# Kernel optimization log

Hardware: AMD Instinct MI355X
Metric: run time of the kernel (lower is better)

Reference implementation:

```python
import jax, jax.numpy as jnp
from jax import lax
import numpy as np

A = 2048          # number of agents
H = 128           # hidden_dim
G = 8             # grid_size
NB = 32.0         # neighbourhood_size
CELL = 2.0 * NB / G


def setup_inputs() -> dict:
    key = jax.random.key(0)
    k1, k2, k3 = jax.random.split(key, 3)
    hidden = jax.random.normal(k1, (A, H), dtype=jnp.float32)
    # positions spread wider than the neighbourhood so bins are exercised
    pos = jax.random.uniform(k2, (A, 2), dtype=jnp.float32, minval=-48.0, maxval=48.0)
    mask = jnp.ones((A,), dtype=bool)
    W = jax.random.normal(k3, (H, G * G * H), dtype=jnp.float32) * (1.0 / np.sqrt(G * G * H))
    b = jnp.zeros((H,), dtype=jnp.float32)
    return {"hidden": hidden, "pos": pos, "mask": mask, "W": W, "b": b}


def reference(hidden, pos, mask, W, b):
    a, h = hidden.shape
    # rel[i, j] = pos[j] - pos[i]  (matches `rel = pos - pos[i]` indexed at j)
    rel = pos[None, :, :] - pos[:, None, :]          # [A, A, 2]
    rx, ry = rel[..., 0], rel[..., 1]
    in_range = (jnp.abs(rx) < NB) & (jnp.abs(ry) < NB)  # also False for NaN rel
    col = jnp.clip(jnp.floor((rx + NB) / CELL).astype(jnp.int32), 0, G - 1)
    row = jnp.clip(jnp.floor((ry + NB) / CELL).astype(jnp.int32), 0, G - 1)
    bins = row * G + col                              # [A, A] in [0, G*G)
    not_self = ~jnp.eye(a, dtype=bool)
    valid = in_range & not_self & mask[None, :]       # [A, A]

    # grid[i, bcell, :] = sum over j with bins[i,j]==bcell of hidden[j]
    def scan_body(_, bcell):
        Mb = (valid & (bins == bcell)).astype(hidden.dtype)   # [A, A]
        return None, Mb @ hidden                              # [A, H]

    _, grid = lax.scan(scan_body, None, jnp.arange(G * G))    # [G*G, A, H]
    grid = jnp.transpose(grid, (1, 0, 2)).reshape(a, G * G * h)
    pooled = grid @ W.T + b                                   # [A, H]

    valid_i = mask & ~jnp.isnan(pos).any(axis=-1)
    return jnp.where(valid_i[:, None], pooled, jnp.zeros_like(pooled))
```

## Files before the change

### kernel.cpp

```cpp
#include <hip/hip_runtime.h>
#include <hip/hip_bf16.h>
#include <stdint.h>


typedef __attribute__((ext_vector_type(4))) float f32x4;
typedef __attribute__((ext_vector_type(8))) short short8;

#define O_HB   0u
#define O_WB   1048576u
#define O_GRID 3145728u
#define O_PART 36700160u
#define O_POSM 36700160u

__device__ __forceinline__ void gl_lds16(const void* g, void* l) {
  __builtin_amdgcn_global_load_lds((const __attribute__((address_space(1))) void*)g,
                                   (__attribute__((address_space(3))) void*)l, 16, 0, 0);
}

__device__ __forceinline__ float bf_lo(uint32_t w) {
  union { uint32_t u; float f; } v{w << 16}; return v.f;
}
__device__ __forceinline__ float bf_hi(uint32_t w) {
  union { uint32_t u; float f; } v{w & 0xffff0000u}; return v.f;
}
__device__ __forceinline__ uint32_t pack_bf2(float x, float y) {
  __hip_bfloat16 bx = __float2bfloat16(x), by = __float2bfloat16(y);
  return ((uint32_t)(*(unsigned short*)&by) << 16) | (*(unsigned short*)&bx);
}

__global__ __launch_bounds__(256) void sp_prep(const float* __restrict__ hidden,
                                               const float* __restrict__ W,
                                               const float* __restrict__ pos,
                                               const int* __restrict__ mask,
                                               __hip_bfloat16* __restrict__ hb,
                                               __hip_bfloat16* __restrict__ wb,
                                               float2* __restrict__ posm) {
  int idx = blockIdx.x * 256 + threadIdx.x;
  const int HID4 = (2049 * 128) / 4;
  const int W4   = (128 * 8192) / 4;
  if (idx < HID4) {
    int e = idx * 4;
    float4 v = make_float4(0.f, 0.f, 0.f, 0.f);
    if (e < 2048 * 128) v = *reinterpret_cast<const float4*>(hidden + e);
    ushort4 pk;
    pk.x = (ushort)(pack_bf2(v.x, v.x) & 0xffffu);
    pk.y = (ushort)(pack_bf2(v.y, v.y) & 0xffffu);
    pk.z = (ushort)(pack_bf2(v.z, v.z) & 0xffffu);
    pk.w = (ushort)(pack_bf2(v.w, v.w) & 0xffffu);
    *reinterpret_cast<ushort4*>(hb + e) = pk;
  } else if (idx < HID4 + W4) {
    int e = (idx - HID4) * 4;
    float4 v = *reinterpret_cast<const float4*>(W + e);
    ushort4 pk;
    pk.x = (ushort)(pack_bf2(v.x, v.x) & 0xffffu);
    pk.y = (ushort)(pack_bf2(v.y, v.y) & 0xffffu);
    pk.z = (ushort)(pack_bf2(v.z, v.z) & 0xffffu);
    pk.w = (ushort)(pack_bf2(v.w, v.w) & 0xffffu);
    *reinterpret_cast<ushort4*>(wb + e) = pk;
  } else {
    int j = idx - (HID4 + W4);
    if (j < 2048) {
      float2 p = reinterpret_cast<const float2*>(pos)[j];
      union { uint32_t u; float f; } qn{0x7fc00000u};
      float2 o;
      bool m = (mask[j] != 0);
      o.x = m ? p.x : qn.f;
      o.y = m ? p.y : qn.f;
      posm[j] = o;
    }
  }
}

__global__ __launch_bounds__(256) void sp_build(const float* __restrict__ pos,
                                                const float2* __restrict__ posm,
                                                const __hip_bfloat16* __restrict__ hb,
                                                __hip_bfloat16* __restrict__ grid) {
  __shared__ __align__(16) uint32_t list32[2560];
  __shared__ int hist[4][64];
  __shared__ int cur[4][64];
  __shared__ int offs[65];
  int t = threadIdx.x;
  int wv = t >> 6;
  int i = blockIdx.x;
  float pxi = pos[2 * i], pyi = pos[2 * i + 1];
  reinterpret_cast<int*>(hist)[t] = 0;
  __syncthreads();
  int bins[8];
  #pragma unroll
  for (int jj = 0; jj < 8; ++jj) {
    int j = t + jj * 256;
    float2 pj = posm[j];
    float rx = pj.x - pxi, ry = pj.y - pyi;
    bool ok = (fabsf(rx) < 32.f) && (fabsf(ry) < 32.f) && (j != i);
    int b = -1;
    if (ok) {
      int col = (int)floorf((rx + 32.f) * 0.125f);
      int row = (int)floorf((ry + 32.f) * 0.125f);
      b = row * 8 + col;
      atomicAdd(&hist[wv][b], 1);
    }
    bins[jj] = b;
  }
  #pragma unroll
  for (int q = 0; q < 10; ++q) {
    int k = t + q * 256;
    if (k < 2560) list32[k] = (2048u << 8);
  }
  __syncthreads();
  if (t < 64) {
    int h0 = hist[0][t], h1 = hist[1][t], h2 = hist[2][t], h3 = hist[3][t];
    int tot = h0 + h1 + h2 + h3;
    int padded = (tot + 7) & ~7;
    int x = padded;
    #pragma unroll
    for (int d = 1; d < 64; d <<= 1) {
      int y = __shfl_up(x, d);
      if (t >= d) x += y;
    }
    offs[t + 1] = x;
    int base = x - padded;
    cur[0][t] = base;
    cur[1][t] = base + h0;
    cur[2][t] = base + h0 + h1;
    cur[3][t] = base + h0 + h1 + h2;
    if (t == 0) offs[0] = 0;
  }
  __syncthreads();
  #pragma unroll
  for (int jj = 0; jj < 8; ++jj) {
    int j = t + jj * 256;
    int b = bins[jj];
    if (b >= 0) { int k = atomicAdd(&cur[wv][b], 1); list32[k] = ((uint32_t)j << 8); }
  }
  __syncthreads();
  int l = t & 63;
  int lq = l & 31;
  int dsh = (l >> 5) << 2;
  int lqoff = lq * 8;
  const char* hbB = reinterpret_cast<const char*>(hb);
  for (int c = wv; c < 64; c += 4) {
    int s0 = offs[c], e0 = offs[c + 1];
    float a0 = 0.f, a1 = 0.f, a2 = 0.f, a3 = 0.f;
    float b0 = 0.f, b1 = 0.f, b2 = 0.f, b3 = 0.f;
    if (s0 < e0) {
      uint4 js = *reinterpret_cast<const uint4*>(&list32[s0 + dsh]);
      uint2 r0 = *reinterpret_cast<const uint2*>(hbB + js.x + lqoff);
      uint2 r1 = *reinterpret_cast<const uint2*>(hbB + js.y + lqoff);
      uint2 r2 = *reinterpret_cast<const uint2*>(hbB + js.z + lqoff);
      uint2 r3 = *reinterpret_cast<const uint2*>(hbB + js.w + lqoff);
      for (int k = s0 + 8; k < e0; k += 8) {
        uint4 jn = *reinterpret_cast<const uint4*>(&list32[k + dsh]);
        uint2 n0 = *reinterpret_cast<const uint2*>(hbB + jn.x + lqoff);
        uint2 n1 = *reinterpret_cast<const uint2*>(hbB + jn.y + lqoff);
        uint2 n2 = *reinterpret_cast<const uint2*>(hbB + jn.z + lqoff);
        uint2 n3 = *reinterpret_cast<const uint2*>(hbB + jn.w + lqoff);
        a0 += bf_lo(r0.x); a1 += bf_hi(r0.x); a2 += bf_lo(r0.y); a3 += bf_hi(r0.y);
        b0 += bf_lo(r1.x); b1 += bf_hi(r1.x); b2 += bf_lo(r1.y); b3 += bf_hi(r1.y);
        a0 += bf_lo(r2.x); a1 += bf_hi(r2.x); a2 += bf_lo(r2.y); a3 += bf_hi(r2.y);
        b0 += bf_lo(r3.x); b1 += bf_hi(r3.x); b2 += bf_lo(r3.y); b3 += bf_hi(r3.y);
        r0 = n0; r1 = n1; r2 = n2; r3 = n3;
      }
      a0 += bf_lo(r0.x); a1 += bf_hi(r0.x); a2 += bf_lo(r0.y); a3 += bf_hi(r0.y);
      b0 += bf_lo(r1.x); b1 += bf_hi(r1.x); b2 += bf_lo(r1.y); b3 += bf_hi(r1.y);
      a0 += bf_lo(r2.x); a1 += bf_hi(r2.x); a2 += bf_lo(r2.y); a3 += bf_hi(r2.y);
      b0 += bf_lo(r3.x); b1 += bf_hi(r3.x); b2 += bf_lo(r3.y); b3 += bf_hi(r3.y);
    }
    float c0 = a0 + b0, c1 = a1 + b1, c2 = a2 + b2, c3 = a3 + b3;
    c0 += __shfl_xor(c0, 32);
    c1 += __shfl_xor(c1, 32);
    c2 += __shfl_xor(c2, 32);
    c3 += __shfl_xor(c3, 32);
    if (l < 32) {
      uint2 pk;
      pk.x = pack_bf2(c0, c1);
      pk.y = pack_bf2(c2, c3);
      *reinterpret_cast<uint2*>(
          reinterpret_cast<char*>(grid) + ((size_t)((i << 6) + c) * 256 + (size_t)lq * 8)) = pk;
    }
  }
}

__global__ __launch_bounds__(256) void sp_gemm(const __hip_bfloat16* __restrict__ Ag,
                                               const __hip_bfloat16* __restrict__ Wb,
                                               float* __restrict__ part) {
  __shared__ __align__(16) char Asm[8192];
  __shared__ __align__(16) char Bsm[16384];
  int t = threadIdx.x;
  int lane = t & 63;
  int w = t >> 6;
  int wm = w >> 1, wn = w & 1;
  int bx = blockIdx.x;
  int mt = bx & 31;
  int sp = bx >> 5;
  int i0 = mt * 64;
  long kbase = (long)sp * 512 * 2;
  const char* Agc = (const char*)Ag;
  const char* Wbc = (const char*)Wb;
  f32x4 acc[2][4] = {};
  for (int st = 0; st < 8; ++st) {
    long kb = kbase + st * 128;
    #pragma unroll
    for (int q = 0; q < 2; ++q) {
      int o = (q * 256 + t) * 16;
      int r = o >> 7;
      int sc = (o & 127) ^ ((r & 7) << 4);
      gl_lds16(Agc + (long)(i0 + r) * 16384 + kb + sc, Asm + o);
    }
    #pragma unroll
    for (int q = 0; q < 4; ++q) {
      int o = (q * 256 + t) * 16;
      int r = o >> 7;
      int sc = (o & 127) ^ ((r & 7) << 4);
      gl_lds16(Wbc + (long)r * 16384 + kb + sc, Bsm + o);
    }
    __syncthreads();
    short8 af[2][2], bfr[4][2];
    #pragma unroll
    for (int fr = 0; fr < 2; ++fr)
      #pragma unroll
      for (int ks = 0; ks < 2; ++ks) {
        int r = wm * 32 + fr * 16 + (lane & 15);
        int g = ks * 4 + (lane >> 4);
        int byt = r * 128 + ((g ^ (r & 7)) << 4);
        af[fr][ks] = *reinterpret_cast<const short8*>(Asm + byt);
      }
    #pragma unroll
    for (int fc = 0; fc < 4; ++fc)
      #pragma unroll
      for (int ks = 0; ks < 2; ++ks) {
        int n = wn * 64 + fc * 16 + (lane & 15);
        int g = ks * 4 + (lane >> 4);
        int byt = n * 128 + ((g ^ (n & 7)) << 4);
        bfr[fc][ks] = *reinterpret_cast<const short8*>(Bsm + byt);
      }
    #pragma unroll
    for (int fr = 0; fr < 2; ++fr)
      #pragma unroll
      for (int fc = 0; fc < 4; ++fc)
        #pragma unroll
        for (int ks = 0; ks < 2; ++ks)
          acc[fr][fc] = __builtin_amdgcn_mfma_f32_16x16x32_bf16(af[fr][ks], bfr[fc][ks],
                                                                acc[fr][fc], 0, 0, 0);
    __syncthreads();
  }
  float* p = part + (long)sp * 262144;
  #pragma unroll
  for (int fr = 0; fr < 2; ++fr)
    #pragma unroll
    for (int fc = 0; fc < 4; ++fc)
      #pragma unroll
      for (int r4 = 0; r4 < 4; ++r4) {
        int ii = i0 + wm * 32 + fr * 16 + (lane >> 4) * 4 + r4;
        int nn = wn * 64 + fc * 16 + (lane & 15);
        p[(long)ii * 128 + nn] = acc[fr][fc][r4];
      }
}

__global__ __launch_bounds__(256) void sp_reduce(const float* __restrict__ part,
                                                 const float* __restrict__ bias,
                                                 const float* __restrict__ pos,
                                                 const int* __restrict__ mask,
                                                 float* __restrict__ out) {
  int g = blockIdx.x * 256 + threadIdx.x;
  int i = g >> 7, n = g & 127;
  float acc = bias[n];
  #pragma unroll
  for (int s = 0; s < 16; ++s) acc += part[(long)s * 262144 + g];
  float px = pos[2 * i], py = pos[2 * i + 1];
  bool vi = (mask[i] != 0) && (px == px) && (py == py);
  out[g] = vi ? acc : 0.f;
}

extern "C" void kernel_launch(void* const* d_in, const int* in_sizes, int n_in,
                              void* d_out, int out_size, void* d_ws, size_t ws_size,
                              hipStream_t stream) {
  const float* hidden  = (const float*)d_in[0];
  const float* pos     = (const float*)d_in[1];
  const int*   mask    = (const int*)d_in[2];
  const float* W       = (const float*)d_in[3];
  const float* bias    = (const float*)d_in[4];
  char* ws = (char*)d_ws;
  __hip_bfloat16* hb   = (__hip_bfloat16*)(ws + O_HB);
  __hip_bfloat16* wb   = (__hip_bfloat16*)(ws + O_WB);
  __hip_bfloat16* grid = (__hip_bfloat16*)(ws + O_GRID);
  float* part          = (float*)(ws + O_PART);
  float2* posm         = (float2*)(ws + O_POSM);
  float* out           = (float*)d_out;

  sp_prep<<<1289, 256, 0, stream>>>(hidden, W, pos, mask, hb, wb, posm);
  sp_build<<<2048, 256, 0, stream>>>(pos, posm, hb, grid);
  sp_gemm<<<512, 256, 0, stream>>>(grid, wb, part);
  sp_reduce<<<1024, 256, 0, stream>>>(part, bias, pos, mask, out);
}
```

Baseline: 67.65 us.

## Give each wavefront one agent with a single streaming pass over per-cell neighbour lists

sp_build now assigns one agent per wavefront (4 agents per block, 512 blocks) instead of one agent per block. Per-wave histograms, prefix scans and 16-bit neighbour lists replace the block-wide shared lists and most __syncthreads. The gather becomes one software-pipelined stream over the whole padded list, flushing a cell whenever a boundary is crossed, so short cells no longer idle the wave. The price is more divergent control flow, a bigger per-wave LDS footprint and serialized boundary handling within each wave.

```diff
diff --git a/kernel.cpp b/kernel.cpp
--- a/kernel.cpp
+++ b/kernel.cpp
@@ -71,112 +71,135 @@
   }
 }
 
+#define FLUSH_CELL()                                                        \
+  {                                                                         \
+    float d0 = a0 + __shfl_xor(a0, 32);                                     \
+    float d1 = a1 + __shfl_xor(a1, 32);                                     \
+    float d2 = a2 + __shfl_xor(a2, 32);                                     \
+    float d3 = a3 + __shfl_xor(a3, 32);                                     \
+    if (loA) {                                                              \
+      uint2 pk; pk.x = pack_bf2(d0, d1); pk.y = pack_bf2(d2, d3);           \
+      *reinterpret_cast<uint2*>(gbase + (c << 8) + laneoff) = pk;           \
+    }                                                                       \
+    a0 = a1 = a2 = a3 = 0.f;                                                \
+  }
+
+#define ISSUE_PAIR(Ldst, sdexpr)                                            \
+  {                                                                         \
+    int sd_ = __builtin_amdgcn_readfirstlane(sdexpr);                       \
+    uint32_t oA_ = (uint32_t)(sd_ & 0xffff) << 8;                           \
+    uint32_t oB_ = ((uint32_t)sd_ >> 16) << 8;                              \
+    uint32_t sel_ = loA ? oA_ : oB_;                                        \
+    Ldst = *reinterpret_cast<const uint2*>(hbB + sel_ + laneoff);           \
+  }
+
+#define ISSUE_BATCH(L, Ea, Eb)                                              \
+  ISSUE_PAIR(L[0], Ea.x) ISSUE_PAIR(L[1], Ea.y)                             \
+  ISSUE_PAIR(L[2], Ea.z) ISSUE_PAIR(L[3], Ea.w)                             \
+  ISSUE_PAIR(L[4], Eb.x) ISSUE_PAIR(L[5], Eb.y)                             \
+  ISSUE_PAIR(L[6], Eb.z) ISSUE_PAIR(L[7], Eb.w)
+
+#define CONSUME_PAIR(Lp)                                                    \
+  {                                                                         \
+    while (c < 64 && rpos == bnd) {                                         \
+      FLUSH_CELL();                                                         \
+      ++c;                                                                  \
+      bnd = (c < 64) ? __builtin_amdgcn_readlane(bndv, c) : 0x7fffffff;     \
+    }                                                                       \
+    uint2 w_ = Lp;                                                          \
+    a0 += bf_lo(w_.x); a1 += bf_hi(w_.x);                                   \
+    a2 += bf_lo(w_.y); a3 += bf_hi(w_.y);                                   \
+    rpos += 2;                                                              \
+  }
+
 __global__ __launch_bounds__(256) void sp_build(const float* __restrict__ pos,
                                                 const float2* __restrict__ posm,
                                                 const __hip_bfloat16* __restrict__ hb,
                                                 __hip_bfloat16* __restrict__ grid) {
-  __shared__ __align__(16) uint32_t list32[2560];
+  __shared__ __align__(16) uint16_t lists[4][2240];
   __shared__ int hist[4][64];
-  __shared__ int cur[4][64];
-  __shared__ int offs[65];
+  __shared__ int curs[4][64];
   int t = threadIdx.x;
   int wv = t >> 6;
-  int i = blockIdx.x;
+  int lane = t & 63;
+  int i = blockIdx.x * 4 + wv;
+  bool loA = lane < 32;
+  uint32_t laneoff = (uint32_t)(lane & 31) * 8;
+
   float pxi = pos[2 * i], pyi = pos[2 * i + 1];
-  reinterpret_cast<int*>(hist)[t] = 0;
-  __syncthreads();
-  int bins[8];
-  #pragma unroll
-  for (int jj = 0; jj < 8; ++jj) {
-    int j = t + jj * 256;
+  hist[wv][lane] = 0;
+  const uint32_t DUMW = 0x08000800u;
+  #pragma unroll
+  for (int q = 0; q < 18; ++q) {
+    int d = lane + q * 64;
+    if (d < 1120) reinterpret_cast<uint32_t*>(lists[wv])[d] = DUMW;
+  }
+  uint32_t bp[8];
+  #pragma unroll
+  for (int r = 0; r < 8; ++r) bp[r] = 0;
+  #pragma unroll
+  for (int ch = 0; ch < 32; ++ch) {
+    int j = ch * 64 + lane;
     float2 pj = posm[j];
     float rx = pj.x - pxi, ry = pj.y - pyi;
     bool ok = (fabsf(rx) < 32.f) && (fabsf(ry) < 32.f) && (j != i);
-    int b = -1;
+    uint32_t b = 255;
     if (ok) {
       int col = (int)floorf((rx + 32.f) * 0.125f);
       int row = (int)floorf((ry + 32.f) * 0.125f);
-      b = row * 8 + col;
+      b = (uint32_t)(row * 8 + col);
       atomicAdd(&hist[wv][b], 1);
     }
-    bins[jj] = b;
-  }
-  #pragma unroll
-  for (int q = 0; q < 10; ++q) {
-    int k = t + q * 256;
-    if (k < 2560) list32[k] = (2048u << 8);
-  }
-  __syncthreads();
-  if (t < 64) {
-    int h0 = hist[0][t], h1 = hist[1][t], h2 = hist[2][t], h3 = hist[3][t];
-    int tot = h0 + h1 + h2 + h3;
-    int padded = (tot + 7) & ~7;
-    int x = padded;
-    #pragma unroll
-    for (int d = 1; d < 64; d <<= 1) {
-      int y = __shfl_up(x, d);
-      if (t >= d) x += y;
-    }
-    offs[t + 1] = x;
-    int base = x - padded;
-    cur[0][t] = base;
-    cur[1][t] = base + h0;
-    cur[2][t] = base + h0 + h1;
-    cur[3][t] = base + h0 + h1 + h2;
-    if (t == 0) offs[0] = 0;
-  }
-  __syncthreads();
-  #pragma unroll
-  for (int jj = 0; jj < 8; ++jj) {
-    int j = t + jj * 256;
-    int b = bins[jj];
-    if (b >= 0) { int k = atomicAdd(&cur[wv][b], 1); list32[k] = ((uint32_t)j << 8); }
-  }
-  __syncthreads();
-  int l = t & 63;
-  int lq = l & 31;
-  int dsh = (l >> 5) << 2;
-  int lqoff = lq * 8;
+    bp[ch >> 2] |= b << ((ch & 3) * 8);
+  }
+  int h = hist[wv][lane];
+  int pc = (h + 1) & ~1;
+  int x = pc;
+  #pragma unroll
+  for (int d = 1; d < 64; d <<= 1) {
+    int y = __shfl_up(x, d);
+    if (lane >= d) x += y;
+  }
+  int bndv = x;
+  curs[wv][lane] = x - pc;
+  int listLen = __builtin_amdgcn_readlane(bndv, 63);
+  #pragma unroll
+  for (int ch = 0; ch < 32; ++ch) {
+    uint32_t b = (bp[ch >> 2] >> ((ch & 3) * 8)) & 255u;
+    if (b != 255u) {
+      int slot = atomicAdd(&curs[wv][b], 1);
+      lists[wv][slot] = (uint16_t)(ch * 64 + lane);
+    }
+  }
+  int Npad = (listLen + 15) & ~15;
+  int nb = Npad >> 4;
   const char* hbB = reinterpret_cast<const char*>(hb);
-  for (int c = wv; c < 64; c += 4) {
-    int s0 = offs[c], e0 = offs[c + 1];
-    float a0 = 0.f, a1 = 0.f, a2 = 0.f, a3 = 0.f;
-    float b0 = 0.f, b1 = 0.f, b2 = 0.f, b3 = 0.f;
-    if (s0 < e0) {
-      uint4 js = *reinterpret_cast<const uint4*>(&list32[s0 + dsh]);
-      uint2 r0 = *reinterpret_cast<const uint2*>(hbB + js.x + lqoff);
-      uint2 r1 = *reinterpret_cast<const uint2*>(hbB + js.y + lqoff);
-      uint2 r2 = *reinterpret_cast<const uint2*>(hbB + js.z + lqoff);
-      uint2 r3 = *reinterpret_cast<const uint2*>(hbB + js.w + lqoff);
-      for (int k = s0 + 8; k < e0; k += 8) {
-        uint4 jn = *reinterpret_cast<const uint4*>(&list32[k + dsh]);
-        uint2 n0 = *reinterpret_cast<const uint2*>(hbB + jn.x + lqoff);
-        uint2 n1 = *reinterpret_cast<const uint2*>(hbB + jn.y + lqoff);
-        uint2 n2 = *reinterpret_cast<const uint2*>(hbB + jn.z + lqoff);
-        uint2 n3 = *reinterpret_cast<const uint2*>(hbB + jn.w + lqoff);
-        a0 += bf_lo(r0.x); a1 += bf_hi(r0.x); a2 += bf_lo(r0.y); a3 += bf_hi(r0.y);
-        b0 += bf_lo(r1.x); b1 += bf_hi(r1.x); b2 += bf_lo(r1.y); b3 += bf_hi(r1.y);
-        a0 += bf_lo(r2.x); a1 += bf_hi(r2.x); a2 += bf_lo(r2.y); a3 += bf_hi(r2.y);
-        b0 += bf_lo(r3.x); b1 += bf_hi(r3.x); b2 += bf_lo(r3.y); b3 += bf_hi(r3.y);
-        r0 = n0; r1 = n1; r2 = n2; r3 = n3;
-      }
-      a0 += bf_lo(r0.x); a1 += bf_hi(r0.x); a2 += bf_lo(r0.y); a3 += bf_hi(r0.y);
-      b0 += bf_lo(r1.x); b1 += bf_hi(r1.x); b2 += bf_lo(r1.y); b3 += bf_hi(r1.y);
-      a0 += bf_lo(r2.x); a1 += bf_hi(r2.x); a2 += bf_lo(r2.y); a3 += bf_hi(r2.y);
-      b0 += bf_lo(r3.x); b1 += bf_hi(r3.x); b2 += bf_lo(r3.y); b3 += bf_hi(r3.y);
-    }
-    float c0 = a0 + b0, c1 = a1 + b1, c2 = a2 + b2, c3 = a3 + b3;
-    c0 += __shfl_xor(c0, 32);
-    c1 += __shfl_xor(c1, 32);
-    c2 += __shfl_xor(c2, 32);
-    c3 += __shfl_xor(c3, 32);
-    if (l < 32) {
-      uint2 pk;
-      pk.x = pack_bf2(c0, c1);
-      pk.y = pack_bf2(c2, c3);
-      *reinterpret_cast<uint2*>(
-          reinterpret_cast<char*>(grid) + ((size_t)((i << 6) + c) * 256 + (size_t)lq * 8)) = pk;
-    }
+  char* gbase = reinterpret_cast<char*>(grid) + ((size_t)i << 14);
+  float a0 = 0.f, a1 = 0.f, a2 = 0.f, a3 = 0.f;
+  int c = 0;
+  int bnd = __builtin_amdgcn_readlane(bndv, 0);
+  int rpos = 0;
+  const char* lw = reinterpret_cast<const char*>(lists[wv]);
+  uint2 Lc[8], Ln[8];
+  int4 E0a = *reinterpret_cast<const int4*>(lw + 0);
+  int4 E0b = *reinterpret_cast<const int4*>(lw + 16);
+  ISSUE_BATCH(Lc, E0a, E0b)
+  int4 EiA = *reinterpret_cast<const int4*>(lw + 32);
+  int4 EiB = *reinterpret_cast<const int4*>(lw + 48);
+  for (int b = 0; b < nb; ++b) {
+    int eoff = (b + 2) * 32;
+    int4 ErA = *reinterpret_cast<const int4*>(lw + eoff);
+    int4 ErB = *reinterpret_cast<const int4*>(lw + eoff + 16);
+    if (b + 1 < nb) { ISSUE_BATCH(Ln, EiA, EiB) }
+    CONSUME_PAIR(Lc[0]) CONSUME_PAIR(Lc[1]) CONSUME_PAIR(Lc[2]) CONSUME_PAIR(Lc[3])
+    CONSUME_PAIR(Lc[4]) CONSUME_PAIR(Lc[5]) CONSUME_PAIR(Lc[6]) CONSUME_PAIR(Lc[7])
+    #pragma unroll
+    for (int p = 0; p < 8; ++p) Lc[p] = Ln[p];
+    EiA = ErA; EiB = ErB;
+  }
+  while (c < 64) {
+    FLUSH_CELL();
+    ++c;
   }
 }
 
@@ -288,7 +311,7 @@
   float* out           = (float*)d_out;
 
   sp_prep<<<1289, 256, 0, stream>>>(hidden, W, pos, mask, hb, wb, posm);
-  sp_build<<<2048, 256, 0, stream>>>(pos, posm, hb, grid);
+  sp_build<<<512, 256, 0, stream>>>(pos, posm, hb, grid);
   sp_gemm<<<512, 256, 0, stream>>>(grid, wb, part);
   sp_reduce<<<1024, 256, 0, stream>>>(part, bias, pos, mask, out);
 }
```

Measured after the change: 92.05 us. 36.1% more time.
